# Kernel tuning notes

Hardware: AMD Instinct MI355X
Metric: run time of the kernel (lower is better)

Reference implementation:

```python
import jax, jax.numpy as jnp
import numpy as np

N = 100000   # num_labels
E = 3200000  # num edges
F_IN, H1, H2 = 384, 128, 64


def setup_inputs() -> dict:
    key = jax.random.key(0)
    k0, k1, k2, k3 = jax.random.split(key, 4)
    x = jax.random.normal(k0, (N, F_IN), dtype=jnp.float32) * 0.05
    W1 = jax.random.normal(k1, (F_IN, H1), dtype=jnp.float32) * (1.0 / np.sqrt(F_IN))
    b1 = jnp.zeros((H1,), dtype=jnp.float32)
    W2 = jax.random.normal(k2, (H1, H2), dtype=jnp.float32) * (1.0 / np.sqrt(H1))
    b2 = jnp.zeros((H2,), dtype=jnp.float32)
    edge_index = jax.random.randint(k3, (2, E), 0, N, dtype=jnp.int32)
    return {"x": x, "W1": W1, "b1": b1, "W2": W2, "b2": b2, "edge_index": edge_index}


def _gcn_norm(edge_index, num_nodes):
    # PyG gcn_norm: add self loops, deg from dst with unit weights, sym norm.
    loops = jnp.arange(num_nodes, dtype=edge_index.dtype)
    src = jnp.concatenate([edge_index[0], loops])
    dst = jnp.concatenate([edge_index[1], loops])
    deg = jax.ops.segment_sum(jnp.ones_like(dst, dtype=jnp.float32), dst,
                              num_segments=num_nodes)
    dis = jnp.where(deg > 0, jax.lax.rsqrt(deg), 0.0)
    norm = dis[src] * dis[dst]  # [E + N]
    return src, dst, norm


def _gcn_conv(x, W, b, src, dst, norm, num_nodes):
    h = x @ W                                   # [N, out]
    msg = h[src] * norm[:, None]                # gather + scale
    out = jax.ops.segment_sum(msg, dst, num_segments=num_nodes)
    return out + b


def reference(x, W1, b1, W2, b2, edge_index):
    src, dst, norm = _gcn_norm(edge_index, N)
    h = jax.nn.relu(_gcn_conv(x, W1, b1, src, dst, norm, N))
    out = _gcn_conv(h, W2, b2, src, dst, norm, N)
    return out
```

## Files before the change

### kernel.cpp

```cpp
#include <hip/hip_runtime.h>
#include <hip/hip_fp16.h>
#include <math.h>

#define N_NODES 100000
#define N_EDGES 3200000
#define F_IN    384
#define H1      128
#define H2      64

#define NBKT    782
#define HIST_W  800
#define NB_BIN  256
#define EPB     (N_EDGES / NB_BIN)

typedef _Float16 f16x8 __attribute__((ext_vector_type(8)));
typedef float    f32x4 __attribute__((ext_vector_type(4)));


__global__ __launch_bounds__(256) void k_hist(const int* __restrict__ dst,
                                              int* __restrict__ hist) {
    __shared__ int h[HIST_W];
    int b = blockIdx.x, t = threadIdx.x;
    for (int i = t; i < HIST_W; i += 256) h[i] = 0;
    __syncthreads();
    int e0 = b * EPB, e1 = e0 + EPB;
    for (int e = e0 + t; e < e1; e += 256)
        atomicAdd(&h[dst[e] >> 7], 1);
    __syncthreads();
    for (int i = t; i < HIST_W; i += 256) hist[b * HIST_W + i] = h[i];
}


__global__ __launch_bounds__(1024) void k_scan_off(int* __restrict__ hist,
                                                   int* __restrict__ bucketBase) {
    __shared__ int s[1024];
    int t = threadIdx.x;
    int run = 0;
    if (t < HIST_W) {
        #pragma unroll 8
        for (int b = 0; b < NB_BIN; b++) {
            int v = hist[b * HIST_W + t];
            hist[b * HIST_W + t] = run;
            run += v;
        }
    }
    int tot = (t < NBKT) ? run : 0;
    s[t] = tot; __syncthreads();
    for (int off = 1; off < 1024; off <<= 1) {
        int x = (t >= off) ? s[t - off] : 0;
        __syncthreads();
        s[t] += x;
        __syncthreads();
    }
    if (t <= NBKT) bucketBase[t] = s[t] - tot;
}


__global__ __launch_bounds__(256) void k_bin(const int* __restrict__ src,
                                             const int* __restrict__ dst,
                                             const int* __restrict__ hist,
                                             const int* __restrict__ bucketBase,
                                             int* __restrict__ binned) {
    __shared__ int lcur[HIST_W];
    int b = blockIdx.x, t = threadIdx.x;
    for (int i = t; i < HIST_W; i += 256)
        lcur[i] = ((i < NBKT) ? bucketBase[i] : 0) + hist[b * HIST_W + i];
    __syncthreads();
    int e0 = b * EPB, e1 = e0 + EPB;
    for (int e = e0 + t; e < e1; e += 256) {
        int d = dst[e];
        int p = atomicAdd(&lcur[d >> 7], 1);
        binned[p] = ((d & 127) << 17) | src[e];
    }
}


__global__ __launch_bounds__(256) void k_build(const int* __restrict__ binned,
                                               const int* __restrict__ bucketBase,
                                               int* __restrict__ csr,
                                               int* __restrict__ offsets,
                                               int* __restrict__ ecnt,
                                               float* __restrict__ dis) {
    __shared__ int ldeg[128], spre[128], lcur[128];
    int bkt = blockIdx.x, t = threadIdx.x;
    int e0 = bucketBase[bkt], e1 = bucketBase[bkt + 1];
    if (t < 128) ldeg[t] = 0;
    __syncthreads();
    for (int e = e0 + t; e < e1; e += 256)
        atomicAdd(&ldeg[binned[e] >> 17], 1);
    __syncthreads();
    int v = (t < 128) ? ldeg[t] : 0;
    if (t < 128) spre[t] = v;
    __syncthreads();
    for (int off = 1; off < 128; off <<= 1) {
        int x = (t < 128 && t >= off) ? spre[t - off] : 0;
        __syncthreads();
        if (t < 128) spre[t] += x;
        __syncthreads();
    }
    if (t < 128) {
        int node = bkt * 128 + t;
        if (node < N_NODES) {
            int base = e0 + spre[t] - v;
            offsets[node] = base;
            ecnt[node]    = v;
            dis[node]     = rsqrtf((float)(v + 1));
            lcur[t]       = base;
        }
    }
    __syncthreads();
    for (int e = e0 + t; e < e1; e += 256) {
        int p = binned[e];
        int pos = atomicAdd(&lcur[p >> 17], 1);
        csr[pos] = p & 0x1FFFF;
    }
}


__global__ __launch_bounds__(256) void k_w1t(const float* __restrict__ W1,
                                             __half* __restrict__ w1t) {
    int id = blockIdx.x * 256 + threadIdx.x;
    int c = id / F_IN, k = id % F_IN;
    w1t[id] = __float2half_rn(W1[(size_t)k * H1 + c]);
}

__global__ __launch_bounds__(256) void k_w2t(const float* __restrict__ W2,
                                             __half* __restrict__ w2t) {
    int id = blockIdx.x * 256 + threadIdx.x;
    int c = id / H1, k = id % H1;
    w2t[id] = __float2half_rn(W2[(size_t)k * H2 + c]);
}


__global__ __launch_bounds__(256) void k_gemm1(const float* __restrict__ x,
                                               const __half* __restrict__ w1t,
                                               const float* __restrict__ dis,
                                               __half* __restrict__ hs1) {
    __shared__ f16x8 xl[512];
    __shared__ f16x8 wt[1024];
    int t = threadIdx.x;
    int m0 = blockIdx.x * 64;
    int wv = t >> 6, l = t & 63;
    int lrow = l & 15, kg = l >> 4;
    f32x4 acc[8];
    #pragma unroll
    for (int nb = 0; nb < 8; nb++) acc[nb] = (f32x4){0.f, 0.f, 0.f, 0.f};

    char* xb = (char*)xl;
    char* wb = (char*)wt;

    for (int k0 = 0; k0 < F_IN; k0 += 64) {
        #pragma unroll
        for (int j = 0; j < 2; j++) {
            int s = t + j * 256;
            int r = s >> 3, kc = (s & 7) * 8;
            int rg = m0 + r; if (rg >= N_NODES) rg = N_NODES - 1;
            const float* px = &x[(size_t)rg * F_IN + k0 + kc];
            float4 p0 = *(const float4*)px;
            float4 p1 = *(const float4*)(px + 4);
            f16x8 h;
            h[0] = (_Float16)p0.x; h[1] = (_Float16)p0.y;
            h[2] = (_Float16)p0.z; h[3] = (_Float16)p0.w;
            h[4] = (_Float16)p1.x; h[5] = (_Float16)p1.y;
            h[6] = (_Float16)p1.z; h[7] = (_Float16)p1.w;
            *(f16x8*)(xb + ((r * 128 + kc * 2) ^ ((r & 7) << 4))) = h;
        }
        #pragma unroll
        for (int j = 0; j < 4; j++) {
            int s = t + j * 256;
            int c = s >> 3, kc = (s & 7) * 8;
            f16x8 h = *(const f16x8*)&w1t[(size_t)c * F_IN + k0 + kc];
            *(f16x8*)(wb + ((c * 128 + kc * 2) ^ ((c & 7) << 4))) = h;
        }
        __syncthreads();
        #pragma unroll
        for (int ks = 0; ks < 2; ks++) {
            int r = wv * 16 + lrow;
            int kb = (ks * 32 + kg * 8) * 2;
            f16x8 a = *(const f16x8*)(xb + ((r * 128 + kb) ^ ((r & 7) << 4)));
            #pragma unroll
            for (int nb = 0; nb < 8; nb++) {
                int c = nb * 16 + lrow;
                f16x8 b = *(const f16x8*)(wb + ((c * 128 + kb) ^ ((c & 7) << 4)));
                acc[nb] = __builtin_amdgcn_mfma_f32_16x16x32_f16(a, b, acc[nb], 0, 0, 0);
            }
        }
        __syncthreads();
    }
    int rbase = m0 + wv * 16 + kg * 4;
    #pragma unroll
    for (int reg = 0; reg < 4; reg++) {
        int row = rbase + reg;
        if (row < N_NODES) {
            float dr = dis[row];
            #pragma unroll
            for (int nb = 0; nb < 8; nb++)
                hs1[(size_t)row * H1 + nb * 16 + lrow] = __float2half_rn(acc[nb][reg] * dr);
        }
    }
}


__global__ __launch_bounds__(256) void k_agg1(const __half* __restrict__ hs1,
                                              const float* __restrict__ dis,
                                              const int* __restrict__ csr,
                                              const int* __restrict__ offsets,
                                              const int* __restrict__ ecnt,
                                              const float* __restrict__ b1,
                                              float* __restrict__ hr) {
    int t = threadIdx.x;
    int w = blockIdx.x * 8 + ((t >> 6) << 1) + ((t & 63) >> 5);
    int fl = t & 31;
    int f4 = fl << 2;
    float di = dis[w];
    int start = offsets[w];
    int cnt = ecnt[w];
    uint2 selfr = *(const uint2*)(hs1 + ((unsigned)w << 7) + f4);
    float2 s0 = __half22float2(*(__half2*)&selfr.x);
    float2 s1 = __half22float2(*(__half2*)&selfr.y);
    float a0 = s0.x, a1 = s0.y, a2 = s1.x, a3 = s1.y;

    int kfull = cnt & ~7;
    for (int k = 0; k < kfull; k += 8) {
        int s[8]; uint2 r[8];
        #pragma unroll
        for (int u = 0; u < 8; u++) s[u] = csr[start + k + u];
        #pragma unroll
        for (int u = 0; u < 8; u++)
            r[u] = *(const uint2*)(hs1 + (((unsigned)s[u] << 7) | f4));
        #pragma unroll
        for (int u = 0; u < 8; u++) {
            float2 f0 = __half22float2(*(__half2*)&r[u].x);
            float2 f1 = __half22float2(*(__half2*)&r[u].y);
            a0 += f0.x; a1 += f0.y; a2 += f1.x; a3 += f1.y;
        }
    }
    for (int k = kfull; k < cnt; k++) {
        int s = csr[start + k];
        uint2 rr = *(const uint2*)(hs1 + (((unsigned)s << 7) | f4));
        float2 f0 = __half22float2(*(__half2*)&rr.x);
        float2 f1 = __half22float2(*(__half2*)&rr.y);
        a0 += f0.x; a1 += f0.y; a2 += f1.x; a3 += f1.y;
    }
    float4 bb = *(const float4*)&b1[f4];
    float4 o = make_float4(fmaxf(bb.x + di * a0, 0.f),
                           fmaxf(bb.y + di * a1, 0.f),
                           fmaxf(bb.z + di * a2, 0.f),
                           fmaxf(bb.w + di * a3, 0.f));
    *(float4*)&hr[((size_t)w << 7) + f4] = o;
}


__global__ __launch_bounds__(256) void k_gemm2(const float* __restrict__ hr,
                                               const __half* __restrict__ w2t,
                                               const float* __restrict__ dis,
                                               __half* __restrict__ hs2) {
    __shared__ f16x8 al[1024];
    __shared__ f16x8 bl[1024];
    int t = threadIdx.x;
    int m0 = blockIdx.x * 64;
    int wv = t >> 6, l = t & 63;
    int lrow = l & 15, kg = l >> 4;
    char* ab = (char*)al;
    char* bb = (char*)bl;

    #pragma unroll
    for (int j = 0; j < 4; j++) {
        int s = t + j * 256;
        int r = s >> 4, kc = (s & 15) * 8;
        int rg = m0 + r; if (rg >= N_NODES) rg = N_NODES - 1;
        const float* ph = &hr[(size_t)rg * H1 + kc];
        float4 p0 = *(const float4*)ph;
        float4 p1 = *(const float4*)(ph + 4);
        f16x8 h;
        h[0] = (_Float16)p0.x; h[1] = (_Float16)p0.y;
        h[2] = (_Float16)p0.z; h[3] = (_Float16)p0.w;
        h[4] = (_Float16)p1.x; h[5] = (_Float16)p1.y;
        h[6] = (_Float16)p1.z; h[7] = (_Float16)p1.w;
        *(f16x8*)(ab + ((r * 256 + kc * 2) ^ ((r & 7) << 4))) = h;
    }
    #pragma unroll
    for (int j = 0; j < 4; j++) {
        int s = t + j * 256;
        int c = s >> 4, kc = (s & 15) * 8;
        f16x8 h = *(const f16x8*)&w2t[(size_t)c * H1 + kc];
        *(f16x8*)(bb + ((c * 256 + kc * 2) ^ ((c & 7) << 4))) = h;
    }
    __syncthreads();

    f32x4 acc[4];
    #pragma unroll
    for (int nb = 0; nb < 4; nb++) acc[nb] = (f32x4){0.f, 0.f, 0.f, 0.f};
    #pragma unroll
    for (int ks = 0; ks < 4; ks++) {
        int r = wv * 16 + lrow;
        int kb = (ks * 32 + kg * 8) * 2;
        f16x8 a = *(const f16x8*)(ab + ((r * 256 + kb) ^ ((r & 7) << 4)));
        #pragma unroll
        for (int nb = 0; nb < 4; nb++) {
            int c = nb * 16 + lrow;
            f16x8 b = *(const f16x8*)(bb + ((c * 256 + kb) ^ ((c & 7) << 4)));
            acc[nb] = __builtin_amdgcn_mfma_f32_16x16x32_f16(a, b, acc[nb], 0, 0, 0);
        }
    }
    int rbase = m0 + wv * 16 + kg * 4;
    #pragma unroll
    for (int reg = 0; reg < 4; reg++) {
        int row = rbase + reg;
        if (row < N_NODES) {
            float dr = dis[row];
            #pragma unroll
            for (int nb = 0; nb < 4; nb++)
                hs2[(size_t)row * H2 + nb * 16 + lrow] = __float2half_rn(acc[nb][reg] * dr);
        }
    }
}


__global__ __launch_bounds__(256) void k_agg2(const __half* __restrict__ hs2,
                                              const float* __restrict__ dis,
                                              const int* __restrict__ csr,
                                              const int* __restrict__ offsets,
                                              const int* __restrict__ ecnt,
                                              const float* __restrict__ b2,
                                              float* __restrict__ out) {
    int t = threadIdx.x;
    int w = blockIdx.x * 16 + ((t >> 6) << 2) + ((t & 63) >> 4);
    int fl = t & 15;
    int f4 = fl << 2;
    float di = dis[w];
    int start = offsets[w];
    int cnt = ecnt[w];
    uint2 selfr = *(const uint2*)(hs2 + ((unsigned)w << 6) + f4);
    float2 s0 = __half22float2(*(__half2*)&selfr.x);
    float2 s1 = __half22float2(*(__half2*)&selfr.y);
    float a0 = s0.x, a1 = s0.y, a2 = s1.x, a3 = s1.y;

    int kfull = cnt & ~7;
    for (int k = 0; k < kfull; k += 8) {
        int s[8]; uint2 r[8];
        #pragma unroll
        for (int u = 0; u < 8; u++) s[u] = csr[start + k + u];
        #pragma unroll
        for (int u = 0; u < 8; u++)
            r[u] = *(const uint2*)(hs2 + (((unsigned)s[u] << 6) | f4));
        #pragma unroll
        for (int u = 0; u < 8; u++) {
            float2 f0 = __half22float2(*(__half2*)&r[u].x);
            float2 f1 = __half22float2(*(__half2*)&r[u].y);
            a0 += f0.x; a1 += f0.y; a2 += f1.x; a3 += f1.y;
        }
    }
    for (int k = kfull; k < cnt; k++) {
        int s = csr[start + k];
        uint2 rr = *(const uint2*)(hs2 + (((unsigned)s << 6) | f4));
        float2 f0 = __half22float2(*(__half2*)&rr.x);
        float2 f1 = __half22float2(*(__half2*)&rr.y);
        a0 += f0.x; a1 += f0.y; a2 += f1.x; a3 += f1.y;
    }
    float4 bb = *(const float4*)&b2[f4];
    float4 o = make_float4(bb.x + di * a0, bb.y + di * a1,
                           bb.z + di * a2, bb.w + di * a3);
    *(float4*)&out[((size_t)w << 6) + f4] = o;
}


extern "C" void kernel_launch(void* const* d_in, const int* in_sizes, int n_in,
                              void* d_out, int out_size, void* d_ws, size_t ws_size,
                              hipStream_t stream) {
    const float* x  = (const float*)d_in[0];
    const float* W1 = (const float*)d_in[1];
    const float* b1 = (const float*)d_in[2];
    const float* W2 = (const float*)d_in[3];
    const float* b2 = (const float*)d_in[4];
    const int*   ei = (const int*)d_in[5];
    const int* src = ei;
    const int* dst = ei + N_EDGES;
    float* out = (float*)d_out;

    char* ws = (char*)d_ws;
    float* dis        = (float*)ws; ws += (size_t)N_NODES * 4;
    int*   offsets    = (int*)ws;   ws += (size_t)N_NODES * 4;
    int*   ecnt       = (int*)ws;   ws += (size_t)N_NODES * 4;
    int*   bucketBase = (int*)ws;   ws += 1024 * 4;
    int*   hist       = (int*)ws;   ws += (size_t)NB_BIN * HIST_W * 4;
    int*   csr        = (int*)ws;   ws += (size_t)N_EDGES * 4;
    __half* w1t       = (__half*)ws; ws += (size_t)H1 * F_IN * 2;
    __half* w2t       = (__half*)ws; ws += (size_t)H2 * H1 * 2;
    __half* hs1       = (__half*)ws; ws += (size_t)N_NODES * H1 * 2;
    float* hr         = (float*)ws; ws += (size_t)N_NODES * H1 * 4;
    int*   binned     = (int*)hr;
    __half* hs2       = hs1;

    k_w1t     <<<(H1 * F_IN) / 256, 256, 0, stream>>>(W1, w1t);
    k_w2t     <<<(H2 * H1) / 256, 256, 0, stream>>>(W2, w2t);
    k_hist    <<<NB_BIN, 256, 0, stream>>>(dst, hist);
    k_scan_off<<<1, 1024, 0, stream>>>(hist, bucketBase);
    k_bin     <<<NB_BIN, 256, 0, stream>>>(src, dst, hist, bucketBase, binned);
    k_build   <<<NBKT, 256, 0, stream>>>(binned, bucketBase, csr, offsets, ecnt, dis);

    k_gemm1<<<(N_NODES + 63) / 64, 256, 0, stream>>>(x, w1t, dis, hs1);
    k_agg1<<<N_NODES / 8, 256, 0, stream>>>(hs1, dis, csr, offsets, ecnt, b1, hr);
    k_gemm2<<<(N_NODES + 63) / 64, 256, 0, stream>>>(hr, w2t, dis, hs2);
    k_agg2<<<N_NODES / 16, 256, 0, stream>>>(hs2, dis, csr, offsets, ecnt, b2, out);
}
```

Baseline: 582.8 us.

## Slab feature layout for aggregations with XCD-mapped slabs, fp16 hidden buffer

The GEMM outputs are now stored as 16-feature slabs (slab-major, node-minor), and each aggregation block processes one slab. The block index's low bits pick the slab, so each XCD's L2 only holds a 3.2 MB slab of the gather table instead of the whole table. The ReLU hidden activations are also written as fp16 rather than fp32, which halves that write and the GEMM2 read. In exchange, the CSR index list is reread once per slab (8x in agg1, 4x in agg2), and fp16 rounding now happens earlier.

```diff
diff --git a/kernel.cpp b/kernel.cpp
--- a/kernel.cpp
+++ b/kernel.cpp
@@ -195,7 +195,8 @@
             float dr = dis[row];
             #pragma unroll
             for (int nb = 0; nb < 8; nb++)
-                hs1[(size_t)row * H1 + nb * 16 + lrow] = __float2half_rn(acc[nb][reg] * dr);
+                hs1[(((size_t)nb * N_NODES + row) << 4) + lrow] =
+                    __float2half_rn(acc[nb][reg] * dr);
         }
     }
 }
@@ -207,27 +208,29 @@
                                               const int* __restrict__ offsets,
                                               const int* __restrict__ ecnt,
                                               const float* __restrict__ b1,
-                                              float* __restrict__ hr) {
+                                              __half* __restrict__ hr16) {
     int t = threadIdx.x;
-    int w = blockIdx.x * 8 + ((t >> 6) << 1) + ((t & 63) >> 5);
-    int fl = t & 31;
-    int f4 = fl << 2;
+    int slab = blockIdx.x & 7;
+    int w = (blockIdx.x >> 3) * 64 + (t >> 2);
+    if (w >= N_NODES) return;
+    int f4 = (t & 3) << 2;
+    const __half* __restrict__ hp = hs1 + (((size_t)slab * N_NODES) << 4);
     float di = dis[w];
     int start = offsets[w];
     int cnt = ecnt[w];
-    uint2 selfr = *(const uint2*)(hs1 + ((unsigned)w << 7) + f4);
-    float2 s0 = __half22float2(*(__half2*)&selfr.x);
-    float2 s1 = __half22float2(*(__half2*)&selfr.y);
+    uint2 r0 = *(const uint2*)(hp + (((unsigned)w) << 4) + f4);
+    float2 s0 = __half22float2(*(__half2*)&r0.x);
+    float2 s1 = __half22float2(*(__half2*)&r0.y);
     float a0 = s0.x, a1 = s0.y, a2 = s1.x, a3 = s1.y;
 
-    int kfull = cnt & ~7;
-    for (int k = 0; k < kfull; k += 8) {
+    int kf = cnt & ~7;
+    for (int k = 0; k < kf; k += 8) {
         int s[8]; uint2 r[8];
         #pragma unroll
         for (int u = 0; u < 8; u++) s[u] = csr[start + k + u];
         #pragma unroll
         for (int u = 0; u < 8; u++)
-            r[u] = *(const uint2*)(hs1 + (((unsigned)s[u] << 7) | f4));
+            r[u] = *(const uint2*)(hp + (((unsigned)s[u]) << 4) + f4);
         #pragma unroll
         for (int u = 0; u < 8; u++) {
             float2 f0 = __half22float2(*(__half2*)&r[u].x);
@@ -235,23 +238,23 @@
             a0 += f0.x; a1 += f0.y; a2 += f1.x; a3 += f1.y;
         }
     }
-    for (int k = kfull; k < cnt; k++) {
+    for (int k = kf; k < cnt; k++) {
         int s = csr[start + k];
-        uint2 rr = *(const uint2*)(hs1 + (((unsigned)s << 7) | f4));
+        uint2 rr = *(const uint2*)(hp + (((unsigned)s) << 4) + f4);
         float2 f0 = __half22float2(*(__half2*)&rr.x);
         float2 f1 = __half22float2(*(__half2*)&rr.y);
         a0 += f0.x; a1 += f0.y; a2 += f1.x; a3 += f1.y;
     }
-    float4 bb = *(const float4*)&b1[f4];
-    float4 o = make_float4(fmaxf(bb.x + di * a0, 0.f),
-                           fmaxf(bb.y + di * a1, 0.f),
-                           fmaxf(bb.z + di * a2, 0.f),
-                           fmaxf(bb.w + di * a3, 0.f));
-    *(float4*)&hr[((size_t)w << 7) + f4] = o;
-}
-
-
-__global__ __launch_bounds__(256) void k_gemm2(const float* __restrict__ hr,
+    int fc = slab * 16 + f4;
+    float4 bb = *(const float4*)&b1[fc];
+    __half2 o0 = __floats2half2_rn(fmaxf(bb.x + di * a0, 0.f), fmaxf(bb.y + di * a1, 0.f));
+    __half2 o1 = __floats2half2_rn(fmaxf(bb.z + di * a2, 0.f), fmaxf(bb.w + di * a3, 0.f));
+    uint2 ov; *(__half2*)&ov.x = o0; *(__half2*)&ov.y = o1;
+    *(uint2*)(hr16 + (((size_t)w) << 7) + fc) = ov;
+}
+
+
+__global__ __launch_bounds__(256) void k_gemm2(const __half* __restrict__ hr16,
                                                const __half* __restrict__ w2t,
                                                const float* __restrict__ dis,
                                                __half* __restrict__ hs2) {
@@ -269,14 +272,7 @@
         int s = t + j * 256;
         int r = s >> 4, kc = (s & 15) * 8;
         int rg = m0 + r; if (rg >= N_NODES) rg = N_NODES - 1;
-        const float* ph = &hr[(size_t)rg * H1 + kc];
-        float4 p0 = *(const float4*)ph;
-        float4 p1 = *(const float4*)(ph + 4);
-        f16x8 h;
-        h[0] = (_Float16)p0.x; h[1] = (_Float16)p0.y;
-        h[2] = (_Float16)p0.z; h[3] = (_Float16)p0.w;
-        h[4] = (_Float16)p1.x; h[5] = (_Float16)p1.y;
-        h[6] = (_Float16)p1.z; h[7] = (_Float16)p1.w;
+        f16x8 h = *(const f16x8*)&hr16[(size_t)rg * H1 + kc];
         *(f16x8*)(ab + ((r * 256 + kc * 2) ^ ((r & 7) << 4))) = h;
     }
     #pragma unroll
@@ -311,7 +307,8 @@
             float dr = dis[row];
             #pragma unroll
             for (int nb = 0; nb < 4; nb++)
-                hs2[(size_t)row * H2 + nb * 16 + lrow] = __float2half_rn(acc[nb][reg] * dr);
+                hs2[(((size_t)nb * N_NODES + row) << 4) + lrow] =
+                    __float2half_rn(acc[nb][reg] * dr);
         }
     }
 }
@@ -325,25 +322,29 @@
                                               const float* __restrict__ b2,
                                               float* __restrict__ out) {
     int t = threadIdx.x;
-    int w = blockIdx.x * 16 + ((t >> 6) << 2) + ((t & 63) >> 4);
-    int fl = t & 15;
-    int f4 = fl << 2;
+    int xcd = blockIdx.x & 7;
+    int slab = xcd >> 1;
+    int chunk = (blockIdx.x >> 3) * 2 + (xcd & 1);
+    int w = chunk * 64 + (t >> 2);
+    if (w >= N_NODES) return;
+    int f4 = (t & 3) << 2;
+    const __half* __restrict__ hp = hs2 + (((size_t)slab * N_NODES) << 4);
     float di = dis[w];
     int start = offsets[w];
     int cnt = ecnt[w];
-    uint2 selfr = *(const uint2*)(hs2 + ((unsigned)w << 6) + f4);
-    float2 s0 = __half22float2(*(__half2*)&selfr.x);
-    float2 s1 = __half22float2(*(__half2*)&selfr.y);
+    uint2 r0 = *(const uint2*)(hp + (((unsigned)w) << 4) + f4);
+    float2 s0 = __half22float2(*(__half2*)&r0.x);
+    float2 s1 = __half22float2(*(__half2*)&r0.y);
     float a0 = s0.x, a1 = s0.y, a2 = s1.x, a3 = s1.y;
 
-    int kfull = cnt & ~7;
-    for (int k = 0; k < kfull; k += 8) {
+    int kf = cnt & ~7;
+    for (int k = 0; k < kf; k += 8) {
         int s[8]; uint2 r[8];
         #pragma unroll
         for (int u = 0; u < 8; u++) s[u] = csr[start + k + u];
         #pragma unroll
         for (int u = 0; u < 8; u++)
-            r[u] = *(const uint2*)(hs2 + (((unsigned)s[u] << 6) | f4));
+            r[u] = *(const uint2*)(hp + (((unsigned)s[u]) << 4) + f4);
         #pragma unroll
         for (int u = 0; u < 8; u++) {
             float2 f0 = __half22float2(*(__half2*)&r[u].x);
@@ -351,17 +352,18 @@
             a0 += f0.x; a1 += f0.y; a2 += f1.x; a3 += f1.y;
         }
     }
-    for (int k = kfull; k < cnt; k++) {
+    for (int k = kf; k < cnt; k++) {
         int s = csr[start + k];
-        uint2 rr = *(const uint2*)(hs2 + (((unsigned)s << 6) | f4));
+        uint2 rr = *(const uint2*)(hp + (((unsigned)s) << 4) + f4);
         float2 f0 = __half22float2(*(__half2*)&rr.x);
         float2 f1 = __half22float2(*(__half2*)&rr.y);
         a0 += f0.x; a1 += f0.y; a2 += f1.x; a3 += f1.y;
     }
-    float4 bb = *(const float4*)&b2[f4];
+    int fc = slab * 16 + f4;
+    float4 bb = *(const float4*)&b2[fc];
     float4 o = make_float4(bb.x + di * a0, bb.y + di * a1,
                            bb.z + di * a2, bb.w + di * a3);
-    *(float4*)&out[((size_t)w << 6) + f4] = o;
+    *(float4*)&out[(((size_t)w) << 6) + fc] = o;
 }
 
 
@@ -388,8 +390,8 @@
     __half* w1t       = (__half*)ws; ws += (size_t)H1 * F_IN * 2;
     __half* w2t       = (__half*)ws; ws += (size_t)H2 * H1 * 2;
     __half* hs1       = (__half*)ws; ws += (size_t)N_NODES * H1 * 2;
-    float* hr         = (float*)ws; ws += (size_t)N_NODES * H1 * 4;
-    int*   binned     = (int*)hr;
+    __half* hr16      = (__half*)ws; ws += (size_t)N_NODES * H1 * 2;
+    int*   binned     = (int*)hr16;
     __half* hs2       = hs1;
 
     k_w1t     <<<(H1 * F_IN) / 256, 256, 0, stream>>>(W1, w1t);
@@ -400,7 +402,7 @@
     k_build   <<<NBKT, 256, 0, stream>>>(binned, bucketBase, csr, offsets, ecnt, dis);
 
     k_gemm1<<<(N_NODES + 63) / 64, 256, 0, stream>>>(x, w1t, dis, hs1);
-    k_agg1<<<N_NODES / 8, 256, 0, stream>>>(hs1, dis, csr, offsets, ecnt, b1, hr);
-    k_gemm2<<<(N_NODES + 63) / 64, 256, 0, stream>>>(hr, w2t, dis, hs2);
-    k_agg2<<<N_NODES / 16, 256, 0, stream>>>(hs2, dis, csr, offsets, ecnt, b2, out);
-}
+    k_agg1<<<((N_NODES + 63) / 64) * 8, 256, 0, stream>>>(hs1, dis, csr, offsets, ecnt, b1, hr16);
+    k_gemm2<<<(N_NODES + 63) / 64, 256, 0, stream>>>(hr16, w2t, dis, hs2);
+    k_agg2<<<((N_NODES + 127) / 128) * 8, 256, 0, stream>>>(hs2, dis, csr, offsets, ecnt, b2, out);
+}
```

Measured after the change: 673.3 us. +15.5%, slower.
